# Kernel tuning notes

Measured on AMD Instinct MI355X. Metric: run time of the kernel, lower is better.

The kernel has to match this reference:

```python
import jax, jax.numpy as jnp
import numpy as np

N, T = 128, 256
QN, QD = 16, 32           # Qn_num, Qn_dim
QL_SIZES = [100] * 8      # Ql category sizes
LD = 32                   # Ql_dim
H = 1024                  # hidden_dim
L = 2                     # layer_num
OUT = 2                   # output_dim
IN_DIM = QN * QD + len(QL_SIZES) * LD  # 768
EPS = 1e-5


def setup_inputs() -> dict:
    key = jax.random.key(0)
    ks = jax.random.split(key, 14)
    qn = jax.random.normal(ks[0], (N, T, QN), dtype=jnp.float32)
    ql = jax.random.randint(ks[1], (N, T, len(QL_SIZES)), 0, 100).astype(jnp.float32)
    x = jnp.concatenate([qn, ql], axis=2)  # [N,T,24]
    std = 1.0 / np.sqrt(H)
    u = lambda k, s: jax.random.uniform(k, s, minval=-std, maxval=std, dtype=jnp.float32)
    return dict(
        x=x,
        QnV=jax.random.normal(ks[2], (QN, QD), dtype=jnp.float32) * 0.5,
        QlV=jax.random.normal(ks[3], (sum(QL_SIZES), LD), dtype=jnp.float32) * 0.5,
        bn_gamma=jnp.ones((QN,), jnp.float32),
        bn_beta=jnp.zeros((QN,), jnp.float32),
        W0=u(ks[4], (IN_DIM + H, 4 * H)), b0=u(ks[5], (4 * H,)),
        W1=u(ks[6], (2 * H, 4 * H)), b1=u(ks[7], (4 * H,)),
        ln_gamma=u(ks[8], (L, 4, H)), ln_beta=u(ks[9], (L, 4, H)),
        fcW=u(ks[10], (H, OUT)), fcb=u(ks[11], (OUT,)),
    )


def _layernorm(v, g, b):
    m = v.mean(-1, keepdims=True)
    s = v.var(-1, keepdims=True)
    return (v - m) * jax.lax.rsqrt(s + EPS) * g + b


def reference(x, QnV, QlV, bn_gamma, bn_beta, W0, b0, W1, b1, ln_gamma, ln_beta, fcW, fcb):
    # ---- data_trans ----
    qn = x[:, :, :QN]                               # [N,T,QN] float features
    ql_idx = x[:, :, QN:].astype(jnp.int32)         # [N,T,Lq] category indices
    offsets = jnp.asarray(np.concatenate([[0], np.cumsum(QL_SIZES)[:-1]]), jnp.int32)
    ql_idx = ql_idx + offsets.reshape(1, 1, -1)
    # BatchNorm1d (training mode): stats over flattened N*T rows, per feature
    flat = qn.reshape(-1, QN)
    mu = flat.mean(0)
    var = flat.var(0)
    qn = (qn - mu) * jax.lax.rsqrt(var + EPS) * bn_gamma + bn_beta
    qn_emb = qn[..., None] * QnV                    # einsum ijk,kd->ijkd : [N,T,QN,QD]
    ql_emb = QlV[ql_idx]                            # [N,T,Lq,LD]
    feats = jnp.concatenate([qn_emb, ql_emb], axis=2).reshape(N, T, IN_DIM)

    Ws, bs = [W0, W1], [b0, b1]

    def step(carry, xt):  # xt: [N, IN_DIM]
        hn, cn = carry     # each [L, N, H]
        xcur = xt
        hs, cs = [], []
        for i in range(L):
            inp = jnp.concatenate([hn[i], xcur], axis=1)
            gates = inp @ Ws[i] + bs[i]             # [N, 4H]
            ig, fg, gg, og = jnp.split(gates, 4, axis=1)
            ig = jax.nn.sigmoid(_layernorm(ig, ln_gamma[i, 0], ln_beta[i, 0]))
            fg = jax.nn.sigmoid(_layernorm(fg, ln_gamma[i, 1], ln_beta[i, 1]))
            gn = _layernorm(gg, ln_gamma[i, 2], ln_beta[i, 2])
            og = jax.nn.sigmoid(_layernorm(og, ln_gamma[i, 3], ln_beta[i, 3]))
            c = cn[i] * fg + ig * jnp.tanh(gn)
            # NOTE: original adds the pre-tanh normalized cellgate (quirk, kept faithful)
            xcur = og * jnp.tanh(c) + gn
            hs.append(xcur)
            cs.append(c)
        return (jnp.stack(hs), jnp.stack(cs)), xcur  # emit last layer h

    h0 = jnp.zeros((L, N, H), jnp.float32)
    c0 = jnp.zeros((L, N, H), jnp.float32)
    xs = jnp.transpose(feats, (1, 0, 2))            # [T, N, IN_DIM]
    _, outs = jax.lax.scan(step, (h0, c0), xs)      # [T, N, H]
    outs = jnp.transpose(outs, (1, 0, 2))           # [N, T, H]
    logits = outs @ fcW + fcb                       # [N, T, OUT]
    return jax.nn.softmax(logits, axis=2)
```

## Files before the change

kernel.cpp:

```cpp
#include <hip/hip_runtime.h>
#include <math.h>


#define N_   128
#define T_   256
#define QN_  16
#define INX  24
#define H_   1024
#define G4   4096
#define FDIM 768
#define EPS_ 1e-5f
#define K0_  1792
#define K1_  2048
#define NSLOT 8
#define HSZ  ((size_t)N_ * H_)
#define SSLOT 16
#define SLSZ (512 * 8 * 16)

typedef unsigned short u16;
typedef unsigned int u32;
typedef unsigned long long u64;
typedef __attribute__((ext_vector_type(8))) short bf16x8;
typedef __attribute__((ext_vector_type(4))) float f32x4;

__device__ __forceinline__ float sigmoidf_(float v) { return 1.0f / (1.0f + expf(-v)); }

__device__ __forceinline__ u16 f2bf(float f) {
  unsigned u = __float_as_uint(f);
  u += 0x7fffu + ((u >> 16) & 1u);
  return (u16)(u >> 16);
}
__device__ __forceinline__ float bf2f(u16 x) {
  return __uint_as_float((u32)x << 16);
}

__device__ __forceinline__ void st_u64g(void* p, u64 v) {
  __hip_atomic_store((u64*)p, v, __ATOMIC_RELAXED, __HIP_MEMORY_SCOPE_AGENT);
}
__device__ __forceinline__ void st_f32g(float* p, float v) {
  __hip_atomic_store(p, v, __ATOMIC_RELAXED, __HIP_MEMORY_SCOPE_AGENT);
}
__device__ __forceinline__ u64 ld_u64g(const void* p) {
  return __hip_atomic_load((const u64*)p, __ATOMIC_RELAXED, __HIP_MEMORY_SCOPE_AGENT);
}
__device__ __forceinline__ void atomAdd_(float* p, float v) {
  __hip_atomic_fetch_add(p, v, __ATOMIC_RELAXED, __HIP_MEMORY_SCOPE_AGENT);
}

__global__ __launch_bounds__(256) void bn_stats_k(const float* __restrict__ x,
    const float* __restrict__ gamma, const float* __restrict__ beta,
    float* __restrict__ scale, float* __restrict__ shift) {
  int q = blockIdx.x;
  int tid = threadIdx.x;
  float s = 0.f, s2 = 0.f;
  for (int r = tid; r < N_ * T_; r += 256) {
    float v = x[(size_t)r * INX + q];
    s += v; s2 += v * v;
  }
  for (int off = 32; off; off >>= 1) { s += __shfl_down(s, off); s2 += __shfl_down(s2, off); }
  __shared__ float red[2][4];
  int w = tid >> 6;
  if ((tid & 63) == 0) { red[0][w] = s; red[1][w] = s2; }
  __syncthreads();
  if (tid == 0) {
    float S = 0.f, S2 = 0.f;
    for (int i = 0; i < 4; ++i) { S += red[0][i]; S2 += red[1][i]; }
    float m   = S  / (float)(N_ * T_);
    float var = S2 / (float)(N_ * T_) - m * m;
    float rs  = rsqrtf(var + EPS_);
    scale[q] = rs * gamma[q];
    shift[q] = beta[q] - m * rs * gamma[q];
  }
}

__global__ __launch_bounds__(256) void feats_all_k(const float* __restrict__ x,
    const float* __restrict__ scale, const float* __restrict__ shift,
    const float* __restrict__ QnV, const float* __restrict__ QlV,
    u16* __restrict__ ft) {
  int rid = blockIdx.x;
  int t = rid >> 7, n = rid & 127;
  const float* xr = x + ((size_t)n * T_ + t) * INX;
  u16* frow = ft + (size_t)rid * FDIM;
  for (int f = threadIdx.x; f < FDIM; f += 256) {
    int d = f & 31;
    float v;
    if (f < 512) {
      int q = f >> 5;
      v = (xr[q] * scale[q] + shift[q]) * QnV[q * 32 + d];
    } else {
      int cg_ = (f - 512) >> 5;
      int idx = (int)xr[QN_ + cg_] + cg_ * 100;
      v = QlV[idx * 32 + d];
    }
    frow[f] = f2bf(v);
  }
}

__global__ __launch_bounds__(256) void wconv_k(const float* __restrict__ W,
                                               u16* __restrict__ WtP, int K) {
  __shared__ u16 L[64][72];
  int tid = threadIdx.x;
  int k0 = blockIdx.x * 64, n0 = blockIdx.y * 64;
#pragma unroll
  for (int it = 0; it < 16; ++it) {
    int e = it * 256 + tid;
    int r = e >> 6, c = e & 63;
    L[r][c] = f2bf(W[(size_t)(k0 + r) * G4 + n0 + c]);
  }
  __syncthreads();
  int n = tid >> 2, ks = (tid & 3) << 4;
  int col = n0 + n;
  int b = (col & 1023) >> 3;
  int j = (col >> 10) * 8 + (col & 7);
  u16* dst = WtP + ((size_t)(b * 32 + j)) * K + k0 + ks;
#pragma unroll
  for (int jj = 0; jj < 16; ++jj) dst[jj] = L[ks + jj][n];
}

#define SUBC(fam, sub) cnts[((fam) * 8 + (sub)) * 16]
#define TOPC(fam)      cnts[(32 + (fam)) * 16]
#define FLAGC(fam)     cnts[(40 + (fam)) * 16]

__device__ __forceinline__ void arrive_tree_(u32* cnts, int fam, int sub, u32 t1) {
  u32 old = __hip_atomic_fetch_add(&SUBC(fam, sub), 1u,
                                   __ATOMIC_RELAXED, __HIP_MEMORY_SCOPE_AGENT);
  if (old == t1 * 16u - 1u) {
    u32 ot = __hip_atomic_fetch_add(&TOPC(fam), 1u,
                                    __ATOMIC_RELAXED, __HIP_MEMORY_SCOPE_AGENT);
    if (ot == t1 * 8u - 1u)
      __hip_atomic_store(&FLAGC(fam), t1, __ATOMIC_RELAXED, __HIP_MEMORY_SCOPE_AGENT);
  }
}
__device__ __forceinline__ void pollflag_(u32* cnts, int fam, u32 t1) {
  while (__hip_atomic_load(&FLAGC(fam), __ATOMIC_RELAXED, __HIP_MEMORY_SCOPE_AGENT) < t1)
    __builtin_amdgcn_s_sleep(1);
}
__device__ __forceinline__ void acqf_(int tid) {
  if (tid < 64) __builtin_amdgcn_fence(__ATOMIC_ACQUIRE, "agent");
  __syncthreads();
}

template<int NS>
__device__ __forceinline__ void gpart(f32x4& a0, f32x4& a1,
    const u16* __restrict__ abase, const u16* __restrict__ wb0,
    const u16* __restrict__ wb1, int cb, int swz, int g) {
#pragma unroll 8
  for (int kc = 0; kc < NS; ++kc) {
    bf16x8 av = *(const bf16x8*)(abase + kc * 32);
    int c = ((cb + kc * 4 + g) ^ swz) << 3;
    bf16x8 bv0 = *(const bf16x8*)(wb0 + c);
    bf16x8 bv1 = *(const bf16x8*)(wb1 + c);
    a0 = __builtin_amdgcn_mfma_f32_16x16x32_bf16(av, bv0, a0, 0, 0, 0);
    a1 = __builtin_amdgcn_mfma_f32_16x16x32_bf16(av, bv1, a1, 0, 0, 0);
  }
}

__device__ __forceinline__ float lnrm2(float v, float2 sq, float g_, float b_) {
  float mean = sq.x * (1.f / (float)H_);
  float var  = sq.y * (1.f / (float)H_) - mean * mean;
  return (v - mean) * rsqrtf(var + EPS_) * g_ + b_;
}

__global__ __launch_bounds__(512, 2) void persist_k(
    const u16* __restrict__ WtP0, const u16* __restrict__ WtP1,
    const u16* __restrict__ ft,
    u16* __restrict__ h0s, u16* __restrict__ h1s,
    const float* __restrict__ b0, const float* __restrict__ b1,
    const float* __restrict__ lng, const float* __restrict__ lnb,
    const float* __restrict__ fcW, const float* __restrict__ fcb,
    float* __restrict__ statsA, float* __restrict__ statsB,
    u32* __restrict__ cnts, float* __restrict__ out) {
  __shared__ u16 wlds[32 * K1_];
  __shared__ float2 sstat[512];
  const int bcu = blockIdx.x, tid = threadIdx.x;
  const int isL0 = bcu < 128;
  const int b    = isL0 ? bcu : bcu - 128;
  const int wave = tid >> 6, lane = tid & 63;
  const int vcol = lane & 15, g4 = lane >> 4;
  const int ga = vcol >> 3, hh = vcol & 7;
  const int swz = vcol & 7;
  const int rowA  = wave * 16 + vcol;
  const int wbase = wave * 16;
  const int sub   = b >> 4;
  const int bank  = b & 7;
  const int hbase = b * 8;
  const int K = isL0 ? K0_ : K1_;

  {
    const u16* wsrc = isL0 ? WtP0 + (size_t)b * 32 * K0_
                           : WtP1 + (size_t)b * 32 * K1_;
    int kc8 = K >> 3;
    for (int cid = tid; cid < 32 * kc8; cid += 512) {
      int j = cid / kc8, ck = cid - j * kc8;
      *(bf16x8*)&wlds[j * K + ((ck ^ (j & 7)) << 3)] =
          *(const bf16x8*)&wsrc[(size_t)j * K + (ck << 3)];
    }
  }
  __syncthreads();
  acqf_(tid);

  const u16* wb0p = &wlds[vcol * K];
  const u16* wb1p = &wlds[(vcol + 16) * K];

  const float* bW   = isL0 ? b0 : b1;
  const float* lngW = isL0 ? lng : lng + 4 * H_;
  const float* lnbW = isL0 ? lnb : lnb + 4 * H_;
  const int colA = ga * H_ + hbase + hh;
  const int colB = (ga + 2) * H_ + hbase + hh;
  const float bias0v = bW[colA], bias1v = bW[colB];
  const float lng0v = lngW[colA], lnb0v = lnbW[colA];
  const float lng1v = lngW[colB], lnb1v = lnbW[colB];
  const float fcb0 = fcb[0], fcb1 = fcb[1];

  float cst[4] = {0.f, 0.f, 0.f, 0.f};

  if (isL0) {
    f32x4 acN0 = {0.f, 0.f, 0.f, 0.f}, acN1 = acN0;
    gpart<24>(acN0, acN1, ft + (size_t)rowA * FDIM + g4 * 8, wb0p, wb1p, 128, swz, g4);

    for (int t = 0; t < T_; ++t) {
      const u32 t1 = (u32)(t + 1);
      u16* h0w = h0s + (size_t)(t & (NSLOT - 1)) * HSZ;
      const u16* h0r = h0s + (size_t)((t - 1) & (NSLOT - 1)) * HSZ;
      float* stA = statsA + (size_t)(t & (SSLOT - 1)) * SLSZ;

      f32x4 ac0 = acN0, ac1 = acN1;
      gpart<32>(ac0, ac1, h0r + (size_t)rowA * H_ + g4 * 8, wb0p, wb1p, 0, swz, g4);
      f32x4 accb0, accb1;
#pragma unroll
      for (int r = 0; r < 4; ++r) { accb0[r] = ac0[r] + bias0v; accb1[r] = ac1[r] + bias1v; }

#pragma unroll
      for (int r = 0; r < 4; ++r) {
        int row = wbase + g4 * 4 + r;
        float s0 = accb0[r], q0 = s0 * s0, s1 = accb1[r], q1 = s1 * s1;
#pragma unroll
        for (int off = 1; off <= 4; off <<= 1) {
          s0 += __shfl_xor(s0, off); q0 += __shfl_xor(q0, off);
          s1 += __shfl_xor(s1, off); q1 += __shfl_xor(q1, off);
        }
        if (hh == 0) {
          float* l0 = &stA[(((row * 4 + ga) * 8) + bank) * 16];
          float* l1 = &stA[(((row * 4 + ga + 2) * 8) + bank) * 16];
          atomAdd_(l0, s0);     atomAdd_(l0 + 1, q0);
          atomAdd_(l1, s1);     atomAdd_(l1 + 1, q1);
        }
      }
      asm volatile("s_waitcnt vmcnt(0)" ::: "memory");
      __syncthreads();
      if (tid == 0) arrive_tree_(cnts, 0, sub, t1);

      {
        float* zs = statsA + (size_t)((t + 8) & (SSLOT - 1)) * SLSZ;
        if (tid < 64) st_f32g(&zs[(b * 32 + (tid >> 1)) * 16 + (tid & 1)], 0.f);
        int tn = (t + 1 < T_) ? t + 1 : t;
        acN0[0] = 0.f; acN0[1] = 0.f; acN0[2] = 0.f; acN0[3] = 0.f;
        acN1 = acN0;
        gpart<24>(acN0, acN1, ft + ((size_t)tn * N_ + rowA) * FDIM + g4 * 8,
                  wb0p, wb1p, 128, swz, g4);
      }
      if (tid == 0) {
        pollflag_(cnts, 0, t1);
        if (t >= 7) pollflag_(cnts, 2, (u32)(t - 6));
      }
      __syncthreads();

      {
        const float* lp = &stA[(size_t)tid * 128];
        float s = 0.f, q = 0.f;
#pragma unroll
        for (int k = 0; k < 8; ++k) {
          u64 v = ld_u64g(lp + k * 16);
          s += __uint_as_float((u32)v);
          q += __uint_as_float((u32)(v >> 32));
        }
        sstat[tid] = make_float2(s, q);
      }
      __syncthreads();

#pragma unroll
      for (int r = 0; r < 4; ++r) {
        int row = wbase + g4 * 4 + r;
        float2 sv0 = sstat[row * 4 + ga];
        float2 sv1 = sstat[row * 4 + ga + 2];
        float nv0 = lnrm2(accb0[r], sv0, lng0v, lnb0v);
        float nv1 = lnrm2(accb1[r], sv1, lng1v, lnb1v);
        float o0 = __shfl_xor(nv0, 8), o1 = __shfl_xor(nv1, 8);
        float vi = ga ? o0 : nv0;
        float vf = ga ? nv0 : o0;
        float vg = ga ? o1 : nv1;
        float vo = ga ? nv1 : o1;
        float igt = sigmoidf_(vi), fgt = sigmoidf_(vf), ogt = sigmoidf_(vo);
        float cn = cst[r] * fgt + igt * tanhf(vg);
        float xn = ogt * tanhf(cn) + vg;
        cst[r] = cn;
        u32 xv = f2bf(xn);
        u32 oth = __shfl_xor((int)xv, 1);
        u32 pr = (hh & 1) ? ((oth & 0xffffu) | (xv << 16)) : ((xv & 0xffffu) | (oth << 16));
        u32 p2 = __shfl_xor((int)pr, 2);
        if (ga == 0 && (hh & 3) == 0)
          st_u64g(&h0w[(size_t)row * H_ + hbase + hh], ((u64)p2 << 32) | pr);
      }
      asm volatile("s_waitcnt vmcnt(0)" ::: "memory");
      __syncthreads();
      if (tid == 0) { arrive_tree_(cnts, 1, sub, t1); pollflag_(cnts, 1, t1); }
      __syncthreads();
      if ((t & (NSLOT - 1)) == NSLOT - 2) acqf_(tid);
    }
  } else {
    for (int t = 0; t < T_; ++t) {
      const u32 t1 = (u32)(t + 1);
      const u16* h0r = h0s + (size_t)(t & (NSLOT - 1)) * HSZ;
      u16* h1w = h1s + (size_t)(t & (NSLOT - 1)) * HSZ;
      const u16* h1r = h1s + (size_t)((t - 1) & (NSLOT - 1)) * HSZ;
      float* stA = statsB + (size_t)(t & (SSLOT - 1)) * SLSZ;

      if (t > 0 && wave == 0) {
        const u16* hrow = h1r + (size_t)b * H_;
        int col = lane * 16;
        bf16x8 v0 = *(const bf16x8*)(hrow + col);
        bf16x8 v1 = *(const bf16x8*)(hrow + col + 8);
        float L0v = 0.f, L1v = 0.f;
#pragma unroll
        for (int j = 0; j < 8; ++j) {
          float x0 = bf2f((u16)v0[j]);
          float2 fw = *(const float2*)&fcW[(col + j) * 2];
          L0v = fmaf(x0, fw.x, L0v); L1v = fmaf(x0, fw.y, L1v);
          float x1 = bf2f((u16)v1[j]);
          float2 fw2 = *(const float2*)&fcW[(col + 8 + j) * 2];
          L0v = fmaf(x1, fw2.x, L0v); L1v = fmaf(x1, fw2.y, L1v);
        }
#pragma unroll
        for (int off = 1; off <= 32; off <<= 1) { L0v += __shfl_xor(L0v, off); L1v += __shfl_xor(L1v, off); }
        if (lane == 0) {
          L0v += fcb0; L1v += fcb1;
          float mx = fmaxf(L0v, L1v);
          float e0 = expf(L0v - mx), e1 = expf(L1v - mx);
          float inv = 1.f / (e0 + e1);
          *(float2*)&out[((size_t)b * T_ + (t - 1)) * 2] = make_float2(e0 * inv, e1 * inv);
        }
      }

      f32x4 ac0 = {0.f, 0.f, 0.f, 0.f}, ac1 = ac0;
      gpart<32>(ac0, ac1, h1r + (size_t)rowA * H_ + g4 * 8, wb0p, wb1p, 0, swz, g4);

      if (tid == 0) pollflag_(cnts, 1, t1);
      __syncthreads();
      gpart<32>(ac0, ac1, h0r + (size_t)rowA * H_ + g4 * 8, wb0p, wb1p, 128, swz, g4);
      f32x4 accb0, accb1;
#pragma unroll
      for (int r = 0; r < 4; ++r) { accb0[r] = ac0[r] + bias0v; accb1[r] = ac1[r] + bias1v; }

#pragma unroll
      for (int r = 0; r < 4; ++r) {
        int row = wbase + g4 * 4 + r;
        float s0 = accb0[r], q0 = s0 * s0, s1 = accb1[r], q1 = s1 * s1;
#pragma unroll
        for (int off = 1; off <= 4; off <<= 1) {
          s0 += __shfl_xor(s0, off); q0 += __shfl_xor(q0, off);
          s1 += __shfl_xor(s1, off); q1 += __shfl_xor(q1, off);
        }
        if (hh == 0) {
          float* l0 = &stA[(((row * 4 + ga) * 8) + bank) * 16];
          float* l1 = &stA[(((row * 4 + ga + 2) * 8) + bank) * 16];
          atomAdd_(l0, s0);     atomAdd_(l0 + 1, q0);
          atomAdd_(l1, s1);     atomAdd_(l1 + 1, q1);
        }
      }
      asm volatile("s_waitcnt vmcnt(0)" ::: "memory");
      __syncthreads();
      if (tid == 0) arrive_tree_(cnts, 2, sub, t1);
      {
        float* zs = statsB + (size_t)((t + 8) & (SSLOT - 1)) * SLSZ;
        if (tid < 64) st_f32g(&zs[(b * 32 + (tid >> 1)) * 16 + (tid & 1)], 0.f);
      }
      if (tid == 0) pollflag_(cnts, 2, t1);
      __syncthreads();

      {
        const float* lp = &stA[(size_t)tid * 128];
        float s = 0.f, q = 0.f;
#pragma unroll
        for (int k = 0; k < 8; ++k) {
          u64 v = ld_u64g(lp + k * 16);
          s += __uint_as_float((u32)v);
          q += __uint_as_float((u32)(v >> 32));
        }
        sstat[tid] = make_float2(s, q);
      }
      __syncthreads();

#pragma unroll
      for (int r = 0; r < 4; ++r) {
        int row = wbase + g4 * 4 + r;
        float2 sv0 = sstat[row * 4 + ga];
        float2 sv1 = sstat[row * 4 + ga + 2];
        float nv0 = lnrm2(accb0[r], sv0, lng0v, lnb0v);
        float nv1 = lnrm2(accb1[r], sv1, lng1v, lnb1v);
        float o0 = __shfl_xor(nv0, 8), o1 = __shfl_xor(nv1, 8);
        float vi = ga ? o0 : nv0;
        float vf = ga ? nv0 : o0;
        float vg = ga ? o1 : nv1;
        float vo = ga ? nv1 : o1;
        float igt = sigmoidf_(vi), fgt = sigmoidf_(vf), ogt = sigmoidf_(vo);
        float cn = cst[r] * fgt + igt * tanhf(vg);
        float xn = ogt * tanhf(cn) + vg;
        cst[r] = cn;
        u32 xv = f2bf(xn);
        u32 oth = __shfl_xor((int)xv, 1);
        u32 pr = (hh & 1) ? ((oth & 0xffffu) | (xv << 16)) : ((xv & 0xffffu) | (oth << 16));
        u32 p2 = __shfl_xor((int)pr, 2);
        if (ga == 0 && (hh & 3) == 0)
          st_u64g(&h1w[(size_t)row * H_ + hbase + hh], ((u64)p2 << 32) | pr);
      }
      asm volatile("s_waitcnt vmcnt(0)" ::: "memory");
      __syncthreads();
      if (tid == 0) { arrive_tree_(cnts, 3, sub, t1); pollflag_(cnts, 3, t1); }
      __syncthreads();
      if ((t & (NSLOT - 1)) == NSLOT - 2) acqf_(tid);
    }
    if (wave == 0) {
      const u16* hrow = h1s + (size_t)((T_ - 1) & (NSLOT - 1)) * HSZ + (size_t)b * H_;
      int col = lane * 16;
      bf16x8 v0 = *(const bf16x8*)(hrow + col);
      bf16x8 v1 = *(const bf16x8*)(hrow + col + 8);
      float L0v = 0.f, L1v = 0.f;
#pragma unroll
      for (int j = 0; j < 8; ++j) {
        float x0 = bf2f((u16)v0[j]);
        float2 fw = *(const float2*)&fcW[(col + j) * 2];
        L0v = fmaf(x0, fw.x, L0v); L1v = fmaf(x0, fw.y, L1v);
        float x1 = bf2f((u16)v1[j]);
        float2 fw2 = *(const float2*)&fcW[(col + 8 + j) * 2];
        L0v = fmaf(x1, fw2.x, L0v); L1v = fmaf(x1, fw2.y, L1v);
      }
#pragma unroll
      for (int off = 1; off <= 32; off <<= 1) { L0v += __shfl_xor(L0v, off); L1v += __shfl_xor(L1v, off); }
      if (lane == 0) {
        L0v += fcb0; L1v += fcb1;
        float mx = fmaxf(L0v, L1v);
        float e0 = expf(L0v - mx), e1 = expf(L1v - mx);
        float inv = 1.f / (e0 + e1);
        *(float2*)&out[((size_t)b * T_ + (T_ - 1)) * 2] = make_float2(e0 * inv, e1 * inv);
      }
    }
  }
}

extern "C" void kernel_launch(void* const* d_in, const int* in_sizes, int n_in,
                              void* d_out, int out_size, void* d_ws, size_t ws_size,
                              hipStream_t stream) {
  const float* x   = (const float*)d_in[0];
  const float* QnV = (const float*)d_in[1];
  const float* QlV = (const float*)d_in[2];
  const float* bng = (const float*)d_in[3];
  const float* bnb = (const float*)d_in[4];
  const float* W0  = (const float*)d_in[5];
  const float* b0  = (const float*)d_in[6];
  const float* W1  = (const float*)d_in[7];
  const float* b1  = (const float*)d_in[8];
  const float* lng = (const float*)d_in[9];
  const float* lnb = (const float*)d_in[10];
  const float* fcW = (const float*)d_in[11];
  const float* fcb = (const float*)d_in[12];
  float* out = (float*)d_out;

  u32*   cnts   = (u32*)d_ws;
  float* statsA = (float*)(cnts + 1024);
  float* statsB = statsA + (size_t)SSLOT * SLSZ;
  u16*   h0s    = (u16*)(statsB + (size_t)SSLOT * SLSZ);
  u16*   h1s    = h0s + (size_t)NSLOT * HSZ;
  size_t zero_bytes = (size_t)((char*)(h1s + (size_t)NSLOT * HSZ) - (char*)d_ws);

  float* scale = (float*)(h1s + (size_t)NSLOT * HSZ);
  float* shift = scale + 64;
  u16* ft   = (u16*)(shift + 64);
  u16* WtP0 = ft + (size_t)N_ * T_ * FDIM;
  u16* WtP1 = WtP0 + (size_t)G4 * K0_;

  hipMemsetAsync(d_ws, 0, zero_bytes, stream);

  bn_stats_k<<<QN_, 256, 0, stream>>>(x, bng, bnb, scale, shift);
  feats_all_k<<<N_ * T_, 256, 0, stream>>>(x, scale, shift, QnV, QlV, ft);
  wconv_k<<<dim3(K0_ / 64, G4 / 64), 256, 0, stream>>>(W0, WtP0, K0_);
  wconv_k<<<dim3(K1_ / 64, G4 / 64), 256, 0, stream>>>(W1, WtP1, K1_);

  void* args[] = {
    (void*)&WtP0, (void*)&WtP1, (void*)&ft, (void*)&h0s, (void*)&h1s,
    (void*)&b0, (void*)&b1, (void*)&lng, (void*)&lnb,
    (void*)&fcW, (void*)&fcb, (void*)&statsA, (void*)&statsB,
    (void*)&cnts, (void*)&out
  };
  hipLaunchCooperativeKernel((void*)persist_k, dim3(256), dim3(512), args, 0, stream);
}
```

Measured before the change: 8.967 ms.

## Replace two-level atomic barrier tree with closer-block polling of sub-counters

The grid barrier no longer uses a second-level top counter. Each block bumps only its sub-counter, and a designated closer block (b==0 or b==1) polls all eight sub-counters in parallel threads before publishing the flag. The intent is to remove one serialized atomic round trip from the critical path of each per-step barrier. In layer 1, the gate GEMM and stats atomics are also moved ahead of the output softmax, so that work overlaps with barrier latency. The cost is extra polling traffic from the closer block and a dependence on which block acts as closer.

```diff
diff --git a/kernel.cpp b/kernel.cpp
--- a/kernel.cpp
+++ b/kernel.cpp
@@ -118,26 +118,35 @@
 }
 
 #define SUBC(fam, sub) cnts[((fam) * 8 + (sub)) * 16]
-#define TOPC(fam)      cnts[(32 + (fam)) * 16]
 #define FLAGC(fam)     cnts[(40 + (fam)) * 16]
 
-__device__ __forceinline__ void arrive_tree_(u32* cnts, int fam, int sub, u32 t1) {
-  u32 old = __hip_atomic_fetch_add(&SUBC(fam, sub), 1u,
-                                   __ATOMIC_RELAXED, __HIP_MEMORY_SCOPE_AGENT);
-  if (old == t1 * 16u - 1u) {
-    u32 ot = __hip_atomic_fetch_add(&TOPC(fam), 1u,
-                                    __ATOMIC_RELAXED, __HIP_MEMORY_SCOPE_AGENT);
-    if (ot == t1 * 8u - 1u)
-      __hip_atomic_store(&FLAGC(fam), t1, __ATOMIC_RELAXED, __HIP_MEMORY_SCOPE_AGENT);
-  }
+__device__ __forceinline__ void arrive_(u32* cnts, int fam, int sub) {
+  __hip_atomic_fetch_add(&SUBC(fam, sub), 1u,
+                         __ATOMIC_RELAXED, __HIP_MEMORY_SCOPE_AGENT);
+}
+__device__ __forceinline__ void pollsub_(u32* cnts, int fam, int sub, u32 tgt16) {
+  while (__hip_atomic_load(&SUBC(fam, sub), __ATOMIC_RELAXED, __HIP_MEMORY_SCOPE_AGENT) < tgt16)
+    __builtin_amdgcn_s_sleep(1);
 }
 __device__ __forceinline__ void pollflag_(u32* cnts, int fam, u32 t1) {
   while (__hip_atomic_load(&FLAGC(fam), __ATOMIC_RELAXED, __HIP_MEMORY_SCOPE_AGENT) < t1)
     __builtin_amdgcn_s_sleep(1);
 }
+__device__ __forceinline__ void stflag_(u32* cnts, int fam, u32 t1) {
+  __hip_atomic_store(&FLAGC(fam), t1, __ATOMIC_RELAXED, __HIP_MEMORY_SCOPE_AGENT);
+}
 __device__ __forceinline__ void acqf_(int tid) {
   if (tid < 64) __builtin_amdgcn_fence(__ATOMIC_ACQUIRE, "agent");
   __syncthreads();
+}
+
+__device__ __forceinline__ void waitfam_(u32* cnts, int fam, u32 t1, int isCloser,
+                                         int tid, int bpFam, u32 bpT1) {
+  if (isCloser) { if (tid < 8) pollsub_(cnts, fam, tid, t1 * 16u); }
+  else          { if (tid == 0) pollflag_(cnts, fam, t1); }
+  if (tid == 8 && bpFam >= 0) pollflag_(cnts, bpFam, bpT1);
+  __syncthreads();
+  if (isCloser && tid == 0) stflag_(cnts, fam, t1);
 }
 
 template<int NS>
@@ -248,7 +257,7 @@
       }
       asm volatile("s_waitcnt vmcnt(0)" ::: "memory");
       __syncthreads();
-      if (tid == 0) arrive_tree_(cnts, 0, sub, t1);
+      if (tid == 0) arrive_(cnts, 0, sub);
 
       {
         float* zs = statsA + (size_t)((t + 8) & (SSLOT - 1)) * SLSZ;
@@ -259,11 +268,8 @@
         gpart<24>(acN0, acN1, ft + ((size_t)tn * N_ + rowA) * FDIM + g4 * 8,
                   wb0p, wb1p, 128, swz, g4);
       }
-      if (tid == 0) {
-        pollflag_(cnts, 0, t1);
-        if (t >= 7) pollflag_(cnts, 2, (u32)(t - 6));
-      }
-      __syncthreads();
+      waitfam_(cnts, 0, t1, b == 0, tid,
+               (t >= 7) ? 2 : -1, (u32)(t - 6));
 
       {
         const float* lp = &stA[(size_t)tid * 128];
@@ -303,8 +309,8 @@
       }
       asm volatile("s_waitcnt vmcnt(0)" ::: "memory");
       __syncthreads();
-      if (tid == 0) { arrive_tree_(cnts, 1, sub, t1); pollflag_(cnts, 1, t1); }
-      __syncthreads();
+      if (tid == 0) arrive_(cnts, 1, sub);
+      waitfam_(cnts, 1, t1, b == 1, tid, -1, 0);
       if ((t & (NSLOT - 1)) == NSLOT - 2) acqf_(tid);
     }
   } else {
@@ -315,6 +321,36 @@
       const u16* h1r = h1s + (size_t)((t - 1) & (NSLOT - 1)) * HSZ;
       float* stA = statsB + (size_t)(t & (SSLOT - 1)) * SLSZ;
 
+      f32x4 ac0 = {0.f, 0.f, 0.f, 0.f}, ac1 = ac0;
+      gpart<32>(ac0, ac1, h1r + (size_t)rowA * H_ + g4 * 8, wb0p, wb1p, 0, swz, g4);
+
+      if (tid == 0) pollflag_(cnts, 1, t1);
+      __syncthreads();
+      gpart<32>(ac0, ac1, h0r + (size_t)rowA * H_ + g4 * 8, wb0p, wb1p, 128, swz, g4);
+      f32x4 accb0, accb1;
+#pragma unroll
+      for (int r = 0; r < 4; ++r) { accb0[r] = ac0[r] + bias0v; accb1[r] = ac1[r] + bias1v; }
+
+#pragma unroll
+      for (int r = 0; r < 4; ++r) {
+        int row = wbase + g4 * 4 + r;
+        float s0 = accb0[r], q0 = s0 * s0, s1 = accb1[r], q1 = s1 * s1;
+#pragma unroll
+        for (int off = 1; off <= 4; off <<= 1) {
+          s0 += __shfl_xor(s0, off); q0 += __shfl_xor(q0, off);
+          s1 += __shfl_xor(s1, off); q1 += __shfl_xor(q1, off);
+        }
+        if (hh == 0) {
+          float* l0 = &stA[(((row * 4 + ga) * 8) + bank) * 16];
+          float* l1 = &stA[(((row * 4 + ga + 2) * 8) + bank) * 16];
+          atomAdd_(l0, s0);     atomAdd_(l0 + 1, q0);
+          atomAdd_(l1, s1);     atomAdd_(l1 + 1, q1);
+        }
+      }
+      asm volatile("s_waitcnt vmcnt(0)" ::: "memory");
+      __syncthreads();
+      if (tid == 0) arrive_(cnts, 2, sub);
+
       if (t > 0 && wave == 0) {
         const u16* hrow = h1r + (size_t)b * H_;
         int col = lane * 16;
@@ -340,42 +376,12 @@
           *(float2*)&out[((size_t)b * T_ + (t - 1)) * 2] = make_float2(e0 * inv, e1 * inv);
         }
       }
-
-      f32x4 ac0 = {0.f, 0.f, 0.f, 0.f}, ac1 = ac0;
-      gpart<32>(ac0, ac1, h1r + (size_t)rowA * H_ + g4 * 8, wb0p, wb1p, 0, swz, g4);
-
-      if (tid == 0) pollflag_(cnts, 1, t1);
-      __syncthreads();
-      gpart<32>(ac0, ac1, h0r + (size_t)rowA * H_ + g4 * 8, wb0p, wb1p, 128, swz, g4);
-      f32x4 accb0, accb1;
-#pragma unroll
-      for (int r = 0; r < 4; ++r) { accb0[r] = ac0[r] + bias0v; accb1[r] = ac1[r] + bias1v; }
-
-#pragma unroll
-      for (int r = 0; r < 4; ++r) {
-        int row = wbase + g4 * 4 + r;
-        float s0 = accb0[r], q0 = s0 * s0, s1 = accb1[r], q1 = s1 * s1;
-#pragma unroll
-        for (int off = 1; off <= 4; off <<= 1) {
-          s0 += __shfl_xor(s0, off); q0 += __shfl_xor(q0, off);
-          s1 += __shfl_xor(s1, off); q1 += __shfl_xor(q1, off);
-        }
-        if (hh == 0) {
-          float* l0 = &stA[(((row * 4 + ga) * 8) + bank) * 16];
-          float* l1 = &stA[(((row * 4 + ga + 2) * 8) + bank) * 16];
-          atomAdd_(l0, s0);     atomAdd_(l0 + 1, q0);
-          atomAdd_(l1, s1);     atomAdd_(l1 + 1, q1);
-        }
-      }
-      asm volatile("s_waitcnt vmcnt(0)" ::: "memory");
-      __syncthreads();
-      if (tid == 0) arrive_tree_(cnts, 2, sub, t1);
       {
         float* zs = statsB + (size_t)((t + 8) & (SSLOT - 1)) * SLSZ;
-        if (tid < 64) st_f32g(&zs[(b * 32 + (tid >> 1)) * 16 + (tid & 1)], 0.f);
-      }
-      if (tid == 0) pollflag_(cnts, 2, t1);
-      __syncthreads();
+        if (tid >= 64 && tid < 128)
+          st_f32g(&zs[(b * 32 + ((tid - 64) >> 1)) * 16 + (tid & 1)], 0.f);
+      }
+      waitfam_(cnts, 2, t1, b == 0, tid, -1, 0);
 
       {
         const float* lp = &stA[(size_t)tid * 128];
@@ -415,8 +421,8 @@
       }
       asm volatile("s_waitcnt vmcnt(0)" ::: "memory");
       __syncthreads();
-      if (tid == 0) { arrive_tree_(cnts, 3, sub, t1); pollflag_(cnts, 3, t1); }
-      __syncthreads();
+      if (tid == 0) arrive_(cnts, 3, sub);
+      waitfam_(cnts, 3, t1, b == 1, tid, -1, 0);
       if ((t & (NSLOT - 1)) == NSLOT - 2) acqf_(tid);
     }
     if (wave == 0) {
```

Measured after the change: 8.512 ms. -5.1%, faster.
